# Kernel optimization log

Hardware: AMD Instinct MI355X
Metric: run time of the kernel (lower is better)

The kernel has to match this reference:

```python
import jax, jax.numpy as jnp
import numpy as np

B, TE, TD, D = 32, 2048, 64, 1024

def setup_inputs() -> dict:
    key = jax.random.key(0)
    k1, k2, k3, k4, k5 = jax.random.split(key, 5)
    return {
        "encoder_outputs": jax.random.normal(k1, (B, TE, D), dtype=jnp.float32),
        "decoder_outputs": jax.random.normal(k2, (B, TD, D), dtype=jnp.float32),
        "W_a": jax.random.normal(k3, (D, D), dtype=jnp.float32) * (1.0 / np.sqrt(D)),
        "U_a": jax.random.normal(k4, (D, D), dtype=jnp.float32) * (1.0 / np.sqrt(D)),
        "V_a": jax.random.normal(k5, (D, 1), dtype=jnp.float32) * (1.0 / np.sqrt(D)),
    }

def reference(encoder_outputs, decoder_outputs, W_a, U_a, V_a):
    # Bahdanau additive attention over encoder positions, query = last decoder step.
    dec_last = decoder_outputs[:, -1, :]                      # [B, D]
    enc_W = jnp.einsum('bte,ef->btf', encoder_outputs, W_a)   # [B, Te, D]
    dec_U = jnp.einsum('bd,df->bf', dec_last, U_a)            # [B, D] (broadcast over Te instead of tile)
    tanh_out = jnp.tanh(enc_W + dec_U[:, None, :])            # [B, Te, D]
    scores = jnp.einsum('btf,fo->bt', tanh_out, V_a[:, 0:1])  # [B, Te] (squeeze of [B,Te,1])
    weights = jax.nn.softmax(scores, axis=1)                  # [B, Te]
    context = jnp.einsum('bte,bt->be', encoder_outputs, weights)  # [B, D]
    return context, weights[..., None]
```

## Files before the change

kernel.cpp:

```cpp
#include <hip/hip_runtime.h>
#include <stdint.h>

#define GLOBAL_AS __attribute__((address_space(1)))
#define LDS_AS    __attribute__((address_space(3)))

typedef __attribute__((ext_vector_type(8))) __bf16 bf16x8;
typedef __attribute__((ext_vector_type(4))) float  f32x4;

__device__ __forceinline__ uint16_t f2b(float f) {
  uint32_t u = __float_as_uint(f);
  u += 0x7fffu + ((u >> 16) & 1u);
  return (uint16_t)(u >> 16);
}
__device__ __forceinline__ float b2f_lo(uint32_t p) { return __uint_as_float(p << 16); }
__device__ __forceinline__ float b2f_hi(uint32_t p) { return __uint_as_float(p & 0xffff0000u); }

#define ASYNC16(gptr, lptr)                                                     \
  __builtin_amdgcn_global_load_lds((GLOBAL_AS void*)(uintptr_t)(gptr),          \
                                   (LDS_AS void*)(lptr), 16, 0, 0)

__global__ __launch_bounds__(256) void convert_enc(const float4* __restrict__ in,
                                                   uint4* __restrict__ out) {
  int i = blockIdx.x * 256 + threadIdx.x;
  float4 a = in[2 * i], b = in[2 * i + 1];
  uint4 o;
  o.x = (uint32_t)f2b(a.x) | ((uint32_t)f2b(a.y) << 16);
  o.y = (uint32_t)f2b(a.z) | ((uint32_t)f2b(a.w) << 16);
  o.z = (uint32_t)f2b(b.x) | ((uint32_t)f2b(b.y) << 16);
  o.w = (uint32_t)f2b(b.z) | ((uint32_t)f2b(b.w) << 16);
  out[i] = o;
}

__global__ __launch_bounds__(256) void convert_WT(const float* __restrict__ W,
                                                  uint16_t* __restrict__ WT) {
  __shared__ float tile[64][65];
  int k0 = (blockIdx.x & 15) * 64;
  int n0 = (blockIdx.x >> 4) * 64;
  #pragma unroll
  for (int it = 0; it < 16; ++it) {
    int idx = it * 256 + threadIdx.x;
    int kr = idx >> 6, nc = idx & 63;
    tile[kr][nc] = W[(size_t)(k0 + kr) * 1024 + n0 + nc];
  }
  __syncthreads();
  #pragma unroll
  for (int it = 0; it < 16; ++it) {
    int idx = it * 256 + threadIdx.x;
    int nr = idx >> 6, kc = idx & 63;
    WT[(size_t)(n0 + nr) * 1024 + k0 + kc] = f2b(tile[kc][nr]);
  }
}

__global__ __launch_bounds__(256) void compute_u(const float* __restrict__ dec,
                                                 const float* __restrict__ U,
                                                 float* __restrict__ u) {
  int b = blockIdx.x >> 2;
  int f = ((blockIdx.x & 3) << 8) + threadIdx.x;
  const float* dl = dec + (size_t)b * 64 * 1024 + 63 * 1024;
  __shared__ float sdec[1024];
  for (int i = threadIdx.x; i < 1024; i += 256) sdec[i] = dl[i];
  __syncthreads();
  float acc = 0.f;
  #pragma unroll 8
  for (int d = 0; d < 1024; ++d) acc = fmaf(sdec[d], U[(size_t)d * 1024 + f], acc);
  u[b * 1024 + f] = acc;
}

__global__ __launch_bounds__(256) void gemm_score(const uint16_t* __restrict__ A,
                                                  const uint16_t* __restrict__ BT,
                                                  const float* __restrict__ u,
                                                  const float* __restrict__ v,
                                                  float* __restrict__ scores) {
  __shared__ __bf16 sA[128 * 32];
  __shared__ __bf16 sB[128 * 32];

  int bx = blockIdx.x;
  int g = bx >> 6, r = bx & 63;
  int mtile = g * 8 + (r & 7);
  int ntile = r >> 3;

  int tid = threadIdx.x;
  int lane = tid & 63;
  int wid  = tid >> 6;
  int wm = (wid & 1) * 64;
  int wn = (wid >> 1) * 64;
  int quad = lane >> 4, nib = lane & 15;

  f32x4 acc[4][4];
  #pragma unroll
  for (int i = 0; i < 4; ++i)
    #pragma unroll
    for (int j = 0; j < 4; ++j) acc[i][j] = (f32x4){0.f, 0.f, 0.f, 0.f};

  const int rowA = mtile * 128;
  const int rowB = ntile * 128;
  const int c0 = tid, c1 = tid + 256;

  for (int k0 = 0; k0 < 1024; k0 += 32) {
    __syncthreads();
    ASYNC16(A  + (size_t)(rowA + (c0 >> 2)) * 1024 + k0 + (c0 & 3) * 8, sA + c0 * 8);
    ASYNC16(A  + (size_t)(rowA + (c1 >> 2)) * 1024 + k0 + (c1 & 3) * 8, sA + c1 * 8);
    ASYNC16(BT + (size_t)(rowB + (c0 >> 2)) * 1024 + k0 + (c0 & 3) * 8, sB + c0 * 8);
    ASYNC16(BT + (size_t)(rowB + (c1 >> 2)) * 1024 + k0 + (c1 & 3) * 8, sB + c1 * 8);
    __syncthreads();

    bf16x8 af[4], bf[4];
    #pragma unroll
    for (int i = 0; i < 4; ++i)
      af[i] = *(const bf16x8*)(sA + (wm + i * 16 + nib) * 32 + quad * 8);
    #pragma unroll
    for (int j = 0; j < 4; ++j)
      bf[j] = *(const bf16x8*)(sB + (wn + j * 16 + nib) * 32 + quad * 8);

    #pragma unroll
    for (int i = 0; i < 4; ++i)
      #pragma unroll
      for (int j = 0; j < 4; ++j)
        acc[i][j] = __builtin_amdgcn_mfma_f32_16x16x32_bf16(af[i], bf[j], acc[i][j], 0, 0, 0);
  }

  int b = rowA >> 11;
  float vv[4], uu[4];
  #pragma unroll
  for (int j = 0; j < 4; ++j) {
    int col = ntile * 128 + wn + j * 16 + nib;
    vv[j] = v[col];
    uu[j] = u[b * 1024 + col];
  }
  #pragma unroll
  for (int i = 0; i < 4; ++i) {
    int rbase = rowA + wm + i * 16 + quad * 4;
    #pragma unroll
    for (int reg = 0; reg < 4; ++reg) {
      float s = 0.f;
      #pragma unroll
      for (int j = 0; j < 4; ++j) s += vv[j] * tanhf(acc[i][j][reg] + uu[j]);
      s += __shfl_xor(s, 1);
      s += __shfl_xor(s, 2);
      s += __shfl_xor(s, 4);
      s += __shfl_xor(s, 8);
      if (nib == 0) atomicAdd(&scores[rbase + reg], s);
    }
  }
}

__global__ __launch_bounds__(256) void softmax_k(const float* __restrict__ scores,
                                                 float* __restrict__ wout) {
  int b = blockIdx.x, tid = threadIdx.x;
  __shared__ float red[4];
  float sv[8];
  float mx = -1e30f;
  #pragma unroll
  for (int i = 0; i < 8; ++i) {
    sv[i] = scores[b * 2048 + i * 256 + tid];
    mx = fmaxf(mx, sv[i]);
  }
  #pragma unroll
  for (int off = 1; off < 64; off <<= 1) mx = fmaxf(mx, __shfl_xor(mx, off));
  if ((tid & 63) == 0) red[tid >> 6] = mx;
  __syncthreads();
  mx = fmaxf(fmaxf(red[0], red[1]), fmaxf(red[2], red[3]));
  __syncthreads();
  float sum = 0.f;
  #pragma unroll
  for (int i = 0; i < 8; ++i) {
    sv[i] = __expf(sv[i] - mx);
    sum += sv[i];
  }
  #pragma unroll
  for (int off = 1; off < 64; off <<= 1) sum += __shfl_xor(sum, off);
  if ((tid & 63) == 0) red[tid >> 6] = sum;
  __syncthreads();
  float inv = 1.0f / (red[0] + red[1] + red[2] + red[3]);
  #pragma unroll
  for (int i = 0; i < 8; ++i) wout[b * 2048 + i * 256 + tid] = sv[i] * inv;
}

__global__ __launch_bounds__(256) void context_k(const uint16_t* __restrict__ encA,
                                                 const float* __restrict__ w,
                                                 float* __restrict__ ctx) {
  int b = blockIdx.x >> 4, ch = blockIdx.x & 15;
  int t0 = ch * 128;
  __shared__ float lw[128];
  if (threadIdx.x < 128) lw[threadIdx.x] = w[b * 2048 + t0 + threadIdx.x];
  __syncthreads();
  int e0 = threadIdx.x * 4;
  float a0 = 0.f, a1 = 0.f, a2 = 0.f, a3 = 0.f;
  const uint16_t* base = encA + (size_t)b * 2048 * 1024 + (size_t)t0 * 1024 + e0;
  #pragma unroll 4
  for (int t = 0; t < 128; ++t) {
    uint2 p = *(const uint2*)(base + (size_t)t * 1024);
    float wt = lw[t];
    a0 = fmaf(wt, b2f_lo(p.x), a0);
    a1 = fmaf(wt, b2f_hi(p.x), a1);
    a2 = fmaf(wt, b2f_lo(p.y), a2);
    a3 = fmaf(wt, b2f_hi(p.y), a3);
  }
  atomicAdd(&ctx[b * 1024 + e0 + 0], a0);
  atomicAdd(&ctx[b * 1024 + e0 + 1], a1);
  atomicAdd(&ctx[b * 1024 + e0 + 2], a2);
  atomicAdd(&ctx[b * 1024 + e0 + 3], a3);
}

extern "C" void kernel_launch(void* const* d_in, const int* in_sizes, int n_in,
                              void* d_out, int out_size, void* d_ws, size_t ws_size,
                              hipStream_t stream) {
  const float* enc = (const float*)d_in[0];
  const float* dec = (const float*)d_in[1];
  const float* Wa  = (const float*)d_in[2];
  const float* Ua  = (const float*)d_in[3];
  const float* Va  = (const float*)d_in[4];

  float* out = (float*)d_out;
  float* ctx = out;
  float* wts = out + 32 * 1024;

  char* ws = (char*)d_ws;
  uint16_t* encA  = (uint16_t*)ws;
  uint16_t* WT    = (uint16_t*)(ws + 134217728);
  float*    ub    = (float*)  (ws + 136314880);
  float*    score = (float*)  (ws + 136445952);

  hipMemsetAsync(ctx, 0, 32 * 1024 * sizeof(float), stream);
  hipMemsetAsync(score, 0, 65536 * sizeof(float), stream);

  convert_enc<<<32768, 256, 0, stream>>>((const float4*)enc, (uint4*)encA);
  convert_WT<<<256, 256, 0, stream>>>(Wa, WT);
  compute_u<<<128, 256, 0, stream>>>(dec, Ua, ub);
  gemm_score<<<4096, 256, 0, stream>>>(encA, WT, ub, Va, score);
  softmax_k<<<32, 256, 0, stream>>>(score, wts);
  context_k<<<512, 256, 0, stream>>>(encA, wts, ctx);
}
```

Measured before the change: 688.2 us.

## Swizzle GEMM LDS layout, fast tanh, deterministic score partials, split-K compute_u

The GEMM's LDS staging is reordered so each 16-row fragment is contiguous, which makes the MFMA operand reads linear per lane and avoids strided LDS access. The library tanhf is replaced with an exp-based formula. Score atomics are replaced by an in-block reduction across the two N-warps plus per-ntile partial buffers that softmax sums. compute_u is split along D with float4 loads and atomics into a zeroed buffer. The exp-based tanh may lose accuracy or overflow to inf for large inputs (it saturates correctly), and softmax now reads 8x more score data.

```diff
diff --git a/kernel.cpp b/kernel.cpp
--- a/kernel.cpp
+++ b/kernel.cpp
@@ -14,6 +14,11 @@
 }
 __device__ __forceinline__ float b2f_lo(uint32_t p) { return __uint_as_float(p << 16); }
 __device__ __forceinline__ float b2f_hi(uint32_t p) { return __uint_as_float(p & 0xffff0000u); }
+
+__device__ __forceinline__ float tanh_fast(float x) {
+  float e = __expf(2.0f * x);
+  return 1.0f - 2.0f / (e + 1.0f);
+}
 
 #define ASYNC16(gptr, lptr)                                                     \
   __builtin_amdgcn_global_load_lds((GLOBAL_AS void*)(uintptr_t)(gptr),          \
@@ -52,27 +57,39 @@
 }
 
 __global__ __launch_bounds__(256) void compute_u(const float* __restrict__ dec,
-                                                 const float* __restrict__ U,
+                                                 const float4* __restrict__ U4,
                                                  float* __restrict__ u) {
-  int b = blockIdx.x >> 2;
-  int f = ((blockIdx.x & 3) << 8) + threadIdx.x;
-  const float* dl = dec + (size_t)b * 64 * 1024 + 63 * 1024;
-  __shared__ float sdec[1024];
-  for (int i = threadIdx.x; i < 1024; i += 256) sdec[i] = dl[i];
-  __syncthreads();
-  float acc = 0.f;
-  #pragma unroll 8
-  for (int d = 0; d < 1024; ++d) acc = fmaf(sdec[d], U[(size_t)d * 1024 + f], acc);
-  u[b * 1024 + f] = acc;
+  int b = blockIdx.x >> 3, dseg = blockIdx.x & 7;
+  __shared__ float sdec[128];
+  if (threadIdx.x < 128)
+    sdec[threadIdx.x] = dec[(size_t)b * 64 * 1024 + 63 * 1024 + dseg * 128 + threadIdx.x];
+  __syncthreads();
+  float4 a = {0.f, 0.f, 0.f, 0.f};
+  const float4* Ub = U4 + (size_t)dseg * 128 * 256 + threadIdx.x;
+  #pragma unroll 4
+  for (int d = 0; d < 128; ++d) {
+    float4 w = Ub[(size_t)d * 256];
+    float s = sdec[d];
+    a.x = fmaf(s, w.x, a.x);
+    a.y = fmaf(s, w.y, a.y);
+    a.z = fmaf(s, w.z, a.z);
+    a.w = fmaf(s, w.w, a.w);
+  }
+  float* up = u + b * 1024 + threadIdx.x * 4;
+  atomicAdd(up + 0, a.x);
+  atomicAdd(up + 1, a.y);
+  atomicAdd(up + 2, a.z);
+  atomicAdd(up + 3, a.w);
 }
 
 __global__ __launch_bounds__(256) void gemm_score(const uint16_t* __restrict__ A,
                                                   const uint16_t* __restrict__ BT,
                                                   const float* __restrict__ u,
                                                   const float* __restrict__ v,
-                                                  float* __restrict__ scores) {
+                                                  float* __restrict__ spart) {
   __shared__ __bf16 sA[128 * 32];
   __shared__ __bf16 sB[128 * 32];
+  __shared__ float sred[128];
 
   int bx = blockIdx.x;
   int g = bx >> 6, r = bx & 63;
@@ -95,22 +112,24 @@
   const int rowA = mtile * 128;
   const int rowB = ntile * 128;
   const int c0 = tid, c1 = tid + 256;
+  const int r0 = ((c0 >> 6) << 4) | (c0 & 15), k0c = ((c0 >> 4) & 3) * 8;
+  const int r1 = ((c1 >> 6) << 4) | (c1 & 15), k1c = ((c1 >> 4) & 3) * 8;
 
   for (int k0 = 0; k0 < 1024; k0 += 32) {
     __syncthreads();
-    ASYNC16(A  + (size_t)(rowA + (c0 >> 2)) * 1024 + k0 + (c0 & 3) * 8, sA + c0 * 8);
-    ASYNC16(A  + (size_t)(rowA + (c1 >> 2)) * 1024 + k0 + (c1 & 3) * 8, sA + c1 * 8);
-    ASYNC16(BT + (size_t)(rowB + (c0 >> 2)) * 1024 + k0 + (c0 & 3) * 8, sB + c0 * 8);
-    ASYNC16(BT + (size_t)(rowB + (c1 >> 2)) * 1024 + k0 + (c1 & 3) * 8, sB + c1 * 8);
+    ASYNC16(A  + (size_t)(rowA + r0) * 1024 + k0 + k0c, sA + c0 * 8);
+    ASYNC16(A  + (size_t)(rowA + r1) * 1024 + k0 + k1c, sA + c1 * 8);
+    ASYNC16(BT + (size_t)(rowB + r0) * 1024 + k0 + k0c, sB + c0 * 8);
+    ASYNC16(BT + (size_t)(rowB + r1) * 1024 + k0 + k1c, sB + c1 * 8);
     __syncthreads();
 
     bf16x8 af[4], bf[4];
     #pragma unroll
     for (int i = 0; i < 4; ++i)
-      af[i] = *(const bf16x8*)(sA + (wm + i * 16 + nib) * 32 + quad * 8);
+      af[i] = *(const bf16x8*)(sA + ((wm >> 4) + i) * 512 + lane * 8);
     #pragma unroll
     for (int j = 0; j < 4; ++j)
-      bf[j] = *(const bf16x8*)(sB + (wn + j * 16 + nib) * 32 + quad * 8);
+      bf[j] = *(const bf16x8*)(sB + ((wn >> 4) + j) * 512 + lane * 8);
 
     #pragma unroll
     for (int i = 0; i < 4; ++i)
@@ -127,24 +146,46 @@
     vv[j] = v[col];
     uu[j] = u[b * 1024 + col];
   }
+  float sloc[4][4];
   #pragma unroll
   for (int i = 0; i < 4; ++i) {
-    int rbase = rowA + wm + i * 16 + quad * 4;
     #pragma unroll
     for (int reg = 0; reg < 4; ++reg) {
       float s = 0.f;
       #pragma unroll
-      for (int j = 0; j < 4; ++j) s += vv[j] * tanhf(acc[i][j][reg] + uu[j]);
+      for (int j = 0; j < 4; ++j) s += vv[j] * tanh_fast(acc[i][j][reg] + uu[j]);
       s += __shfl_xor(s, 1);
       s += __shfl_xor(s, 2);
       s += __shfl_xor(s, 4);
       s += __shfl_xor(s, 8);
-      if (nib == 0) atomicAdd(&scores[rbase + reg], s);
+      sloc[i][reg] = s;
     }
   }
-}
-
-__global__ __launch_bounds__(256) void softmax_k(const float* __restrict__ scores,
+  if (wid < 2) {
+    if (nib == 0) {
+      #pragma unroll
+      for (int i = 0; i < 4; ++i)
+        #pragma unroll
+        for (int reg = 0; reg < 4; ++reg)
+          sred[wm + i * 16 + quad * 4 + reg] = sloc[i][reg];
+    }
+  }
+  __syncthreads();
+  if (wid >= 2 && nib == 0) {
+    float* outp = spart + (size_t)ntile * 65536 + rowA;
+    #pragma unroll
+    for (int i = 0; i < 4; ++i) {
+      int rloc = wm + i * 16 + quad * 4;
+      float4 sv;
+      #pragma unroll
+      for (int reg = 0; reg < 4; ++reg)
+        ((float*)&sv)[reg] = sloc[i][reg] + sred[rloc + reg];
+      *(float4*)(outp + rloc) = sv;
+    }
+  }
+}
+
+__global__ __launch_bounds__(256) void softmax_k(const float* __restrict__ spart,
                                                  float* __restrict__ wout) {
   int b = blockIdx.x, tid = threadIdx.x;
   __shared__ float red[4];
@@ -152,8 +193,12 @@
   float mx = -1e30f;
   #pragma unroll
   for (int i = 0; i < 8; ++i) {
-    sv[i] = scores[b * 2048 + i * 256 + tid];
-    mx = fmaxf(mx, sv[i]);
+    int idx = b * 2048 + i * 256 + tid;
+    float s = 0.f;
+    #pragma unroll
+    for (int j = 0; j < 8; ++j) s += spart[j * 65536 + idx];
+    sv[i] = s;
+    mx = fmaxf(mx, s);
   }
   #pragma unroll
   for (int off = 1; off < 64; off <<= 1) mx = fmaxf(mx, __shfl_xor(mx, off));
@@ -219,15 +264,15 @@
   uint16_t* encA  = (uint16_t*)ws;
   uint16_t* WT    = (uint16_t*)(ws + 134217728);
   float*    ub    = (float*)  (ws + 136314880);
-  float*    score = (float*)  (ws + 136445952);
+  float*    spart = (float*)  (ws + 136445952);
 
   hipMemsetAsync(ctx, 0, 32 * 1024 * sizeof(float), stream);
-  hipMemsetAsync(score, 0, 65536 * sizeof(float), stream);
+  hipMemsetAsync(ub, 0, 32 * 1024 * sizeof(float), stream);
 
   convert_enc<<<32768, 256, 0, stream>>>((const float4*)enc, (uint4*)encA);
   convert_WT<<<256, 256, 0, stream>>>(Wa, WT);
-  compute_u<<<128, 256, 0, stream>>>(dec, Ua, ub);
-  gemm_score<<<4096, 256, 0, stream>>>(encA, WT, ub, Va, score);
-  softmax_k<<<32, 256, 0, stream>>>(score, wts);
+  compute_u<<<256, 256, 0, stream>>>(dec, (const float4*)Ua, ub);
+  gemm_score<<<4096, 256, 0, stream>>>(encA, WT, ub, Va, spart);
+  softmax_k<<<32, 256, 0, stream>>>(spart, wts);
   context_k<<<512, 256, 0, stream>>>(encA, wts, ctx);
 }
```

Result: no change. 698.2 us (+1.5%).
